# Kernel tuning notes

Measured on AMD Instinct MI355X. Metric: run time of the kernel, lower is better.

Reference implementation:

```python
import jax, jax.numpy as jnp
import numpy as np

TWO_PI = 2.0 * np.pi
SIGMA = 25.0  # marginal_prob_std sigma


def marginal_prob_std(t):
    # std(t) = sqrt((sigma^{2t} - 1) / (2 ln sigma)) for VE-SDE
    return jnp.sqrt((SIGMA ** (2.0 * t) - 1.0) / (2.0 * np.log(SIGMA)))


def edge_conv(x, src, dst, W1, b1, W2, b2, num_nodes):
    # PyG EdgeConv: msg = mlp(cat([x_i, x_j - x_i])), x_i = x[dst], x_j = x[src];
    # scatter-max over dst. First linear split so concat is never materialized:
    # cat([x_i, x_j - x_i]) @ W1 = x_i @ (Wa - Wb) + x_j @ Wb
    d = x.shape[-1]
    Wa, Wb = W1[:d], W1[d:]
    h_center = x @ (Wa - Wb)        # [N, H]
    h_nbr = x @ Wb                  # [N, H]
    e = jax.nn.relu(h_center[dst] + h_nbr[src] + b1)  # [E, H]
    e = e @ W2 + b2                 # [E, out]
    return jax.ops.segment_max(e, dst, num_segments=num_nodes)


def setup_inputs() -> dict:
    N, E, B, H, EM = 50000, 500000, 1024, 128, 64
    CLS, SD, GD, WD = 10, 4, 2, 2
    key = jax.random.key(0)
    ks = jax.random.split(key, 32)

    def lin(k, fi, fo):
        return jax.random.normal(k, (fi, fo), jnp.float32) / np.sqrt(fi)

    inp = {
        "t": jax.random.uniform(ks[0], (N, 1), jnp.float32, 1e-3, 1.0),
        "obj_x": jax.random.normal(ks[1], (N, SD), jnp.float32),
        "obj_geo": jax.random.normal(ks[2], (N, GD), jnp.float32),
        "wall": jax.random.normal(ks[3], (B, WD), jnp.float32),
        "category": jax.random.randint(ks[4], (N,), 0, CLS),
        "batch_idx": jnp.sort(jax.random.randint(ks[5], (N,), 0, B)),
        "src": jax.random.randint(ks[6], (E,), 0, N),
        "dst": jnp.tile(jnp.arange(N), E // N),  # every node receives edges
        "embed_W": jax.random.normal(ks[7], (CLS, EM), jnp.float32),
        "gfp_W": jax.random.normal(ks[8], (EM // 2,), jnp.float32) * 30.0,
        "sW": lin(ks[9], EM, EM), "sb": jnp.zeros((EM,), jnp.float32),
        "w1": lin(ks[10], WD, EM), "wb1": jnp.zeros((EM,), jnp.float32),
        "w2": lin(ks[11], EM, EM), "wb2": jnp.zeros((EM,), jnp.float32),
        "i1": lin(ks[12], SD + GD, H), "ib1": jnp.zeros((H,), jnp.float32),
        "i2": lin(ks[13], H, H), "ib2": jnp.zeros((H,), jnp.float32),
        "m1W1": lin(ks[14], 2 * (H + 3 * EM), H), "m1b1": jnp.zeros((H,), jnp.float32),
        "m1W2": lin(ks[15], H, H), "m1b2": jnp.zeros((H,), jnp.float32),
        "m2W1": lin(ks[16], 2 * (H + 3 * EM), H), "m2b1": jnp.zeros((H,), jnp.float32),
        "m2W2": lin(ks[17], H, SD), "m2b2": jnp.zeros((SD,), jnp.float32),
    }
    return inp


def reference(t, obj_x, obj_geo, wall, category, batch_idx, src, dst,
              embed_W, gfp_W, sW, sb, w1, wb1, w2, wb2,
              i1, ib1, i2, ib2, m1W1, m1b1, m1W2, m1b2,
              m2W1, m2b1, m2W2, m2b2):
    N = obj_x.shape[0]
    # conditioning features
    class_feat = jax.nn.relu(embed_W[category])                       # [N, EM]
    tv = t[:, 0]                                                      # [N]
    x_proj = tv[:, None] * gfp_W[None, :] * TWO_PI                    # [N, EM/2]
    gfp = jnp.concatenate([jnp.sin(x_proj), jnp.cos(x_proj)], axis=-1)
    sigma_feat = jax.nn.relu(gfp @ sW + sb)                           # [N, EM]
    wall_h = jax.nn.relu(jax.nn.relu(wall @ w1 + wb1) @ w2 + wb2)     # [B, EM]
    wall_feat = wall_h[batch_idx]                                     # [N, EM]
    cond = jnp.concatenate([class_feat, sigma_feat, wall_feat], axis=-1)

    # init encoder
    xin = jnp.concatenate([obj_x, obj_geo], axis=-1)                  # [N, 6]
    init = jax.nn.relu(jax.nn.relu(xin @ i1 + ib1) @ i2 + ib2)        # [N, H]

    # main backbone: two EdgeConvs with conditioning concat
    x = jnp.concatenate([init, cond], axis=-1)                        # [N, H+3EM]
    x = jax.nn.relu(edge_conv(x, src, dst, m1W1, m1b1, m1W2, m1b2, N))
    x = jnp.concatenate([x, cond], axis=-1)                           # [N, H+3EM]
    x = edge_conv(x, src, dst, m2W1, m2b1, m2W2, m2b2, N)             # [N, 4]

    return x / (marginal_prob_std(t) + 1e-7)
```

## Files before the change

kernel.cpp:

```cpp
#include <hip/hip_runtime.h>
#include <math.h>

#define NTHREADS 256
#define TWO_PI_F 6.28318530717958647692f
#define LOG_SIGMA 3.2188758248682006f

typedef unsigned short u16;
typedef unsigned int u32;
typedef short bf16x8 __attribute__((ext_vector_type(8)));
typedef float f32x4 __attribute__((ext_vector_type(4)));

#define MFMA(a, b, c) __builtin_amdgcn_mfma_f32_16x16x32_bf16((a), (b), (c), 0, 0, 0)

__device__ __forceinline__ u16 f2b(float f) {
  u32 u = __float_as_uint(f);
  u32 r = (u + 0x7fffu + ((u >> 16) & 1u)) >> 16;
  return (u16)r;
}
__device__ __forceinline__ float blo(u32 u) { return __uint_as_float(u << 16); }
__device__ __forceinline__ float bhi(u32 u) { return __uint_as_float(u & 0xffff0000u); }
__device__ __forceinline__ u32 pk(float lo, float hi) { return (u32)f2b(lo) | ((u32)f2b(hi) << 16); }

__global__ __launch_bounds__(256) void prep_kernel(
    const float* __restrict__ m1W2, const float* __restrict__ m1W1,
    const float* __restrict__ m2W1, const float* __restrict__ sW,
    const float* __restrict__ i1, const float* __restrict__ i2,
    u16* __restrict__ m1W2t, u16* __restrict__ Wc1t, u16* __restrict__ Wc2t,
    u16* __restrict__ sWt, u16* __restrict__ i1t, u16* __restrict__ i2t) {
  int idx = blockIdx.x * 256 + threadIdx.x;
  if (idx < 16384) {
    int n = idx >> 7, k = idx & 127;
    m1W2t[idx] = f2b(m1W2[k * 128 + n]);
  } else if (idx < 98304) {
    int j = idx - 16384;
    int n = j / 320, k = j - n * 320;
    float v = (n < 128) ? (m1W1[k * 128 + n] - m1W1[(320 + k) * 128 + n])
                        : m1W1[(320 + k) * 128 + (n - 128)];
    Wc1t[j] = f2b(v);
  } else if (idx < 180224) {
    int j = idx - 98304;
    int n = j / 320, k = j - n * 320;
    float v = (n < 128) ? (m2W1[k * 128 + n] - m2W1[(320 + k) * 128 + n])
                        : m2W1[(320 + k) * 128 + (n - 128)];
    Wc2t[j] = f2b(v);
  } else if (idx < 184320) {
    int j = idx - 180224;
    int n = j >> 6, k = j & 63;
    sWt[j] = f2b(sW[k * 64 + n]);
  } else if (idx < 188416) {
    int j = idx - 184320;
    int n = j >> 5, k = j & 31;
    i1t[j] = (k < 6) ? f2b(i1[k * 128 + n]) : (u16)0;
  } else if (idx < 204800) {
    int j = idx - 188416;
    int n = j >> 7, k = j & 127;
    i2t[j] = f2b(i2[k * 128 + n]);
  }
}

__global__ void wall_kernel(const float* __restrict__ wall,
                            const float* __restrict__ w1, const float* __restrict__ wb1,
                            const float* __restrict__ w2, const float* __restrict__ wb2,
                            float* __restrict__ wall_h) {
  __shared__ float h1[64];
  int b = blockIdx.x;
  int f = threadIdx.x;
  float v = wall[b * 2 + 0] * w1[f] + wall[b * 2 + 1] * w1[64 + f] + wb1[f];
  h1[f] = fmaxf(v, 0.f);
  __syncthreads();
  float acc = wb2[f];
  for (int k = 0; k < 64; ++k) acc = fmaf(h1[k], w2[k * 64 + f], acc);
  wall_h[b * 64 + f] = fmaxf(acc, 0.f);
}

__global__ __launch_bounds__(256) void node_kernel(
    const float* __restrict__ t, const float* __restrict__ obj_x,
    const float* __restrict__ obj_geo,
    const int* __restrict__ category, const int* __restrict__ batch_idx,
    const float* __restrict__ embed_W, const float* __restrict__ gfp_W,
    const u16* __restrict__ sWt, const float* __restrict__ sb,
    const u16* __restrict__ i1t, const float* __restrict__ ib1,
    const u16* __restrict__ i2t, const float* __restrict__ ib2,
    const u16* __restrict__ Wc1t, const float* __restrict__ m1b1,
    const float* __restrict__ wall_h,
    float* __restrict__ hc1, u16* __restrict__ hn1,
    u16* __restrict__ cond_bf, int N) {
  __shared__ u16 xb[64 * 328];
  __shared__ u16 ab[64 * 136];
  __shared__ float t_s[64];
  __shared__ int cat_s[64];
  __shared__ int bid_s[64];

  const int tid = threadIdx.x;
  const int base = blockIdx.x * 64;
  const int wave = tid >> 6, lane = tid & 63;
  const int ln16 = lane & 15, q8 = lane >> 4;

  bf16x8 bs0 = *(const bf16x8*)(sWt + (size_t)((wave * 16 + ln16) * 64) + q8 * 8);
  bf16x8 bs1 = *(const bf16x8*)(sWt + (size_t)((wave * 16 + ln16) * 64) + 32 + q8 * 8);
  bf16x8 bh[2];
#pragma unroll
  for (int nt = 0; nt < 2; ++nt)
    bh[nt] = *(const bf16x8*)(i1t + (size_t)((wave * 32 + nt * 16 + ln16) * 32) + q8 * 8);

  if (tid < 64) {
    int node = min(base + tid, N - 1);
    t_s[tid] = t[node];
    cat_s[tid] = category[node];
    bid_s[tid] = batch_idx[node];
  }
  __syncthreads();

  for (int idx = tid; idx < 64 * 32; idx += NTHREADS) {
    int row = idx >> 5, k = idx & 31;
    float xp = t_s[row] * gfp_W[k] * TWO_PI_F;
    float s, c;
    sincosf(xp, &s, &c);
    ab[row * 136 + k] = f2b(s);
    ab[row * 136 + 32 + k] = f2b(c);
  }
  for (int idx = tid; idx < 64 * 64; idx += NTHREADS) {
    int row = idx >> 6, f = idx & 63;
    xb[row * 328 + 128 + f] = f2b(fmaxf(embed_W[cat_s[row] * 64 + f], 0.f));
    xb[row * 328 + 256 + f] = f2b(wall_h[bid_s[row] * 64 + f]);
  }
  __syncthreads();

  f32x4 cs[4];
#pragma unroll
  for (int mt = 0; mt < 4; ++mt) cs[mt] = (f32x4)0.f;
#pragma unroll
  for (int mt = 0; mt < 4; ++mt) {
    bf16x8 a0 = *(const bf16x8*)&ab[(mt * 16 + ln16) * 136 + q8 * 8];
    cs[mt] = MFMA(a0, bs0, cs[mt]);
  }
#pragma unroll
  for (int mt = 0; mt < 4; ++mt) {
    bf16x8 a1 = *(const bf16x8*)&ab[(mt * 16 + ln16) * 136 + 32 + q8 * 8];
    cs[mt] = MFMA(a1, bs1, cs[mt]);
  }
  __syncthreads();

  {
    int col = wave * 16 + ln16;
    float bias = sb[col];
#pragma unroll
    for (int mt = 0; mt < 4; ++mt)
#pragma unroll
      for (int r = 0; r < 4; ++r)
        xb[(mt * 16 + q8 * 4 + r) * 328 + 192 + col] = f2b(fmaxf(cs[mt][r] + bias, 0.f));
  }
  for (int idx = tid; idx < 64 * 32; idx += NTHREADS) {
    int row = idx >> 5, k = idx & 31;
    int node = min(base + row, N - 1);
    float v = (k < 4) ? obj_x[node * 4 + k] : ((k < 6) ? obj_geo[node * 2 + (k - 4)] : 0.f);
    ab[row * 136 + k] = f2b(v);
  }
  __syncthreads();

  for (int idx = tid; idx < 64 * 24; idx += NTHREADS) {
    int row = idx / 24, q = idx - row * 24;
    int node = base + row;
    if (node < N)
      *(uint4*)&cond_bf[(size_t)node * 192 + q * 8] = *(uint4*)&xb[row * 328 + 128 + q * 8];
  }

  f32x4 ch[2][4];
#pragma unroll
  for (int nt = 0; nt < 2; ++nt)
#pragma unroll
    for (int mt = 0; mt < 4; ++mt) ch[nt][mt] = (f32x4)0.f;
#pragma unroll
  for (int mt = 0; mt < 4; ++mt) {
    bf16x8 a = *(const bf16x8*)&ab[(mt * 16 + ln16) * 136 + q8 * 8];
#pragma unroll
    for (int nt = 0; nt < 2; ++nt) ch[nt][mt] = MFMA(a, bh[nt], ch[nt][mt]);
  }
  bf16x8 bcur2[2], bnext2[2];
#pragma unroll
  for (int nt = 0; nt < 2; ++nt)
    bcur2[nt] = *(const bf16x8*)(i2t + (size_t)((wave * 32 + nt * 16 + ln16) * 128) + q8 * 8);
  __syncthreads();
#pragma unroll
  for (int nt = 0; nt < 2; ++nt) {
    int col = wave * 32 + nt * 16 + ln16;
    float bias = ib1[col];
#pragma unroll
    for (int mt = 0; mt < 4; ++mt)
#pragma unroll
      for (int r = 0; r < 4; ++r)
        ab[(mt * 16 + q8 * 4 + r) * 136 + col] = f2b(fmaxf(ch[nt][mt][r] + bias, 0.f));
  }
  __syncthreads();

  f32x4 ci[2][4];
#pragma unroll
  for (int nt = 0; nt < 2; ++nt)
#pragma unroll
    for (int mt = 0; mt < 4; ++mt) ci[nt][mt] = (f32x4)0.f;
  for (int kt = 0; kt < 4; ++kt) {
    if (kt < 3) {
#pragma unroll
      for (int nt = 0; nt < 2; ++nt)
        bnext2[nt] = *(const bf16x8*)(i2t + (size_t)((wave * 32 + nt * 16 + ln16) * 128) +
                                      (kt + 1) * 32 + q8 * 8);
    }
#pragma unroll
    for (int mt = 0; mt < 4; ++mt) {
      bf16x8 a = *(const bf16x8*)&ab[(mt * 16 + ln16) * 136 + kt * 32 + q8 * 8];
#pragma unroll
      for (int nt = 0; nt < 2; ++nt) ci[nt][mt] = MFMA(a, bcur2[nt], ci[nt][mt]);
    }
#pragma unroll
    for (int nt = 0; nt < 2; ++nt) bcur2[nt] = bnext2[nt];
  }
#pragma unroll
  for (int nt = 0; nt < 2; ++nt) {
    int col = wave * 32 + nt * 16 + ln16;
    float bias = ib2[col];
#pragma unroll
    for (int mt = 0; mt < 4; ++mt)
#pragma unroll
      for (int r = 0; r < 4; ++r)
        xb[(mt * 16 + q8 * 4 + r) * 328 + col] = f2b(fmaxf(ci[nt][mt][r] + bias, 0.f));
  }
  __syncthreads();

  f32x4 c2[4][4];
#pragma unroll
  for (int nt = 0; nt < 4; ++nt)
#pragma unroll
    for (int mt = 0; mt < 4; ++mt) c2[nt][mt] = (f32x4)0.f;
  bf16x8 bcur[4], bnext[4];
#pragma unroll
  for (int nt = 0; nt < 4; ++nt)
    bcur[nt] = *(const bf16x8*)(Wc1t + (size_t)((wave * 64 + nt * 16 + ln16) * 320) + q8 * 8);
  for (int kt = 0; kt < 10; ++kt) {
    if (kt < 9) {
#pragma unroll
      for (int nt = 0; nt < 4; ++nt)
        bnext[nt] = *(const bf16x8*)(Wc1t + (size_t)((wave * 64 + nt * 16 + ln16) * 320) +
                                     (kt + 1) * 32 + q8 * 8);
    }
#pragma unroll
    for (int mt = 0; mt < 4; ++mt) {
      bf16x8 a = *(const bf16x8*)&xb[(mt * 16 + ln16) * 328 + kt * 32 + q8 * 8];
#pragma unroll
      for (int nt = 0; nt < 4; ++nt) c2[nt][mt] = MFMA(a, bcur[nt], c2[nt][mt]);
    }
#pragma unroll
    for (int nt = 0; nt < 4; ++nt) bcur[nt] = bnext[nt];
  }
#pragma unroll
  for (int nt = 0; nt < 4; ++nt) {
    int col = wave * 64 + nt * 16 + ln16;
#pragma unroll
    for (int mt = 0; mt < 4; ++mt)
#pragma unroll
      for (int r = 0; r < 4; ++r) {
        int node = base + mt * 16 + q8 * 4 + r;
        if (node < N) {
          if (col < 128)
            hc1[(size_t)node * 128 + col] = c2[nt][mt][r] + m1b1[col];
          else
            hn1[(size_t)node * 128 + (col - 128)] = f2b(c2[nt][mt][r]);
        }
      }
  }
}

__global__ __launch_bounds__(256) void edge1_kernel(
    const float* __restrict__ hc1, const u16* __restrict__ hn1,
    const u16* __restrict__ cond_bf, const int* __restrict__ src,
    const u16* __restrict__ m1W2t, const float* __restrict__ m1b2,
    const u16* __restrict__ Wc2t, const float* __restrict__ m2b1,
    float* __restrict__ hc2, u16* __restrict__ hn2, int N) {
  __shared__ u16 a_lds[32 * 136];
  __shared__ u16 x2_lds[32 * 328];
  __shared__ int sid[320];

  const int tid = threadIdx.x;
  const int base = blockIdx.x * 32;
  const int wave = tid >> 6, lane = tid & 63;
  const int ln16 = lane & 15, q8 = lane >> 4;

  for (int idx = tid; idx < 320; idx += NTHREADS) {
    int e = idx >> 5, n = idx & 31;
    int node = min(base + n, N - 1);
    sid[idx] = src[node + e * N];
  }
  for (int idx = tid; idx < 768; idx += NTHREADS) {
    int n = idx / 24, q = idx - n * 24;
    int node = min(base + n, N - 1);
    *(uint4*)&x2_lds[n * 328 + 128 + q * 8] = *(const uint4*)&cond_bf[(size_t)node * 192 + q * 8];
  }
  const int ln = tid >> 3, kq = tid & 7;
  const int lnode = min(base + ln, N - 1);
  float hcr[16];
#pragma unroll
  for (int q = 0; q < 4; ++q) {
    float4 v = *(const float4*)&hc1[(size_t)lnode * 128 + kq * 16 + q * 4];
    hcr[q * 4 + 0] = v.x; hcr[q * 4 + 1] = v.y; hcr[q * 4 + 2] = v.z; hcr[q * 4 + 3] = v.w;
  }
  bf16x8 bfrag[2][4];
#pragma unroll
  for (int nt = 0; nt < 2; ++nt)
#pragma unroll
    for (int kt = 0; kt < 4; ++kt)
      bfrag[nt][kt] = *(const bf16x8*)(m1W2t + (size_t)((2 * wave + nt) * 16 + ln16) * 128 +
                                       kt * 32 + q8 * 8);

  f32x4 ymax[2][2];
#pragma unroll
  for (int mt = 0; mt < 2; ++mt)
#pragma unroll
    for (int nt = 0; nt < 2; ++nt)
#pragma unroll
      for (int r = 0; r < 4; ++r) ymax[mt][nt][r] = -3.0e38f;

  __syncthreads();

  int s = sid[ln];
  uint4 g0 = *(const uint4*)&hn1[(size_t)s * 128 + kq * 16];
  uint4 g1 = *(const uint4*)&hn1[(size_t)s * 128 + kq * 16 + 8];

  for (int e = 0; e < 10; ++e) {
    float a[16];
    a[0] = blo(g0.x); a[1] = bhi(g0.x); a[2] = blo(g0.y); a[3] = bhi(g0.y);
    a[4] = blo(g0.z); a[5] = bhi(g0.z); a[6] = blo(g0.w); a[7] = bhi(g0.w);
    a[8] = blo(g1.x); a[9] = bhi(g1.x); a[10] = blo(g1.y); a[11] = bhi(g1.y);
    a[12] = blo(g1.z); a[13] = bhi(g1.z); a[14] = blo(g1.w); a[15] = bhi(g1.w);
#pragma unroll
    for (int i = 0; i < 16; ++i) a[i] = fmaxf(hcr[i] + a[i], 0.f);
    uint4 o0, o1;
    o0.x = pk(a[0], a[1]); o0.y = pk(a[2], a[3]); o0.z = pk(a[4], a[5]); o0.w = pk(a[6], a[7]);
    o1.x = pk(a[8], a[9]); o1.y = pk(a[10], a[11]); o1.z = pk(a[12], a[13]); o1.w = pk(a[14], a[15]);
    *(uint4*)&a_lds[ln * 136 + kq * 16] = o0;
    *(uint4*)&a_lds[ln * 136 + kq * 16 + 8] = o1;
    if (e < 9) {
      s = sid[(e + 1) * 32 + ln];
      g0 = *(const uint4*)&hn1[(size_t)s * 128 + kq * 16];
      g1 = *(const uint4*)&hn1[(size_t)s * 128 + kq * 16 + 8];
    }
    __syncthreads();
    f32x4 c[2][2];
#pragma unroll
    for (int mt = 0; mt < 2; ++mt)
#pragma unroll
      for (int nt = 0; nt < 2; ++nt) c[mt][nt] = (f32x4)0.f;
#pragma unroll
    for (int kt = 0; kt < 4; ++kt) {
      bf16x8 a0 = *(const bf16x8*)&a_lds[ln16 * 136 + kt * 32 + q8 * 8];
      bf16x8 a1 = *(const bf16x8*)&a_lds[(16 + ln16) * 136 + kt * 32 + q8 * 8];
#pragma unroll
      for (int nt = 0; nt < 2; ++nt) {
        c[0][nt] = MFMA(a0, bfrag[nt][kt], c[0][nt]);
        c[1][nt] = MFMA(a1, bfrag[nt][kt], c[1][nt]);
      }
    }
#pragma unroll
    for (int mt = 0; mt < 2; ++mt)
#pragma unroll
      for (int nt = 0; nt < 2; ++nt)
#pragma unroll
        for (int r = 0; r < 4; ++r) ymax[mt][nt][r] = fmaxf(ymax[mt][nt][r], c[mt][nt][r]);
    __syncthreads();
  }

#pragma unroll
  for (int mt = 0; mt < 2; ++mt)
#pragma unroll
    for (int nt = 0; nt < 2; ++nt) {
      int col = (2 * wave + nt) * 16 + ln16;
      float bias = m1b2[col];
#pragma unroll
      for (int r = 0; r < 4; ++r) {
        int row = mt * 16 + q8 * 4 + r;
        x2_lds[row * 328 + col] = f2b(fmaxf(ymax[mt][nt][r] + bias, 0.f));
      }
    }
  __syncthreads();

  f32x4 c2[2][4];
#pragma unroll
  for (int mt = 0; mt < 2; ++mt)
#pragma unroll
    for (int nt = 0; nt < 4; ++nt) c2[mt][nt] = (f32x4)0.f;
  bf16x8 bcur[4], bnext[4];
#pragma unroll
  for (int nt = 0; nt < 4; ++nt)
    bcur[nt] = *(const bf16x8*)(Wc2t + (size_t)((wave * 4 + nt) * 16 + ln16) * 320 + q8 * 8);
  for (int kt = 0; kt < 10; ++kt) {
    if (kt < 9) {
#pragma unroll
      for (int nt = 0; nt < 4; ++nt)
        bnext[nt] = *(const bf16x8*)(Wc2t + (size_t)((wave * 4 + nt) * 16 + ln16) * 320 +
                                     (kt + 1) * 32 + q8 * 8);
    }
    bf16x8 a0 = *(const bf16x8*)&x2_lds[ln16 * 328 + kt * 32 + q8 * 8];
    bf16x8 a1 = *(const bf16x8*)&x2_lds[(16 + ln16) * 328 + kt * 32 + q8 * 8];
#pragma unroll
    for (int nt = 0; nt < 4; ++nt) {
      c2[0][nt] = MFMA(a0, bcur[nt], c2[0][nt]);
      c2[1][nt] = MFMA(a1, bcur[nt], c2[1][nt]);
    }
#pragma unroll
    for (int nt = 0; nt < 4; ++nt) bcur[nt] = bnext[nt];
  }
#pragma unroll
  for (int mt = 0; mt < 2; ++mt)
#pragma unroll
    for (int nt = 0; nt < 4; ++nt) {
      int col = (wave * 4 + nt) * 16 + ln16;
#pragma unroll
      for (int r = 0; r < 4; ++r) {
        int row = mt * 16 + q8 * 4 + r;
        int node = base + row;
        if (node < N) {
          if (wave < 2)
            hc2[(size_t)node * 128 + col] = c2[mt][nt][r] + m2b1[col];
          else
            hn2[(size_t)node * 128 + (col - 128)] = f2b(c2[mt][nt][r]);
        }
      }
    }
}

__global__ __launch_bounds__(256) void edge2_kernel(
    const float* __restrict__ hc2, const u16* __restrict__ hn2,
    const int* __restrict__ src, const float* __restrict__ t,
    const float* __restrict__ m2W2, const float* __restrict__ m2b2,
    float* __restrict__ out, int N) {
  const int tid = threadIdx.x;
  const int base = blockIdx.x * 32;
  const int ln = tid >> 3, kq = tid & 7;
  const int node = min(base + ln, N - 1);

  float hcr[16];
#pragma unroll
  for (int q = 0; q < 4; ++q) {
    float4 v = *(const float4*)&hc2[(size_t)node * 128 + kq * 16 + q * 4];
    hcr[q * 4 + 0] = v.x; hcr[q * 4 + 1] = v.y; hcr[q * 4 + 2] = v.z; hcr[q * 4 + 3] = v.w;
  }
  float w[16][4];
#pragma unroll
  for (int i = 0; i < 16; ++i) {
    float4 v = *(const float4*)&m2W2[(kq * 16 + i) * 4];
    w[i][0] = v.x; w[i][1] = v.y; w[i][2] = v.z; w[i][3] = v.w;
  }
  float ymax[4] = {-3.0e38f, -3.0e38f, -3.0e38f, -3.0e38f};

  int s = src[node];
  uint4 g0 = *(const uint4*)&hn2[(size_t)s * 128 + kq * 16];
  uint4 g1 = *(const uint4*)&hn2[(size_t)s * 128 + kq * 16 + 8];
  for (int e = 0; e < 10; ++e) {
    float a[16];
    a[0] = blo(g0.x); a[1] = bhi(g0.x); a[2] = blo(g0.y); a[3] = bhi(g0.y);
    a[4] = blo(g0.z); a[5] = bhi(g0.z); a[6] = blo(g0.w); a[7] = bhi(g0.w);
    a[8] = blo(g1.x); a[9] = bhi(g1.x); a[10] = blo(g1.y); a[11] = bhi(g1.y);
    a[12] = blo(g1.z); a[13] = bhi(g1.z); a[14] = blo(g1.w); a[15] = bhi(g1.w);
    if (e < 9) {
      s = src[node + (e + 1) * N];
      g0 = *(const uint4*)&hn2[(size_t)s * 128 + kq * 16];
      g1 = *(const uint4*)&hn2[(size_t)s * 128 + kq * 16 + 8];
    }
    float acc[4] = {0.f, 0.f, 0.f, 0.f};
#pragma unroll
    for (int i = 0; i < 16; ++i) {
      float av = fmaxf(hcr[i] + a[i], 0.f);
#pragma unroll
      for (int j = 0; j < 4; ++j) acc[j] = fmaf(av, w[i][j], acc[j]);
    }
#pragma unroll
    for (int mask = 1; mask <= 4; mask <<= 1)
#pragma unroll
      for (int j = 0; j < 4; ++j) acc[j] += __shfl_xor(acc[j], mask);
#pragma unroll
    for (int j = 0; j < 4; ++j) ymax[j] = fmaxf(ymax[j], acc[j]);
  }
  if (kq < 4 && base + ln < N) {
    float tv = t[node];
    float mps = sqrtf((expf(2.f * tv * LOG_SIGMA) - 1.f) * (1.f / (2.f * LOG_SIGMA)));
    out[(size_t)node * 4 + kq] = (ymax[kq] + m2b2[kq]) / (mps + 1e-7f);
  }
}

extern "C" void kernel_launch(void* const* d_in, const int* in_sizes, int n_in,
                              void* d_out, int out_size, void* d_ws, size_t ws_size,
                              hipStream_t stream) {
  const float* t = (const float*)d_in[0];
  const float* obj_x = (const float*)d_in[1];
  const float* obj_geo = (const float*)d_in[2];
  const float* wall = (const float*)d_in[3];
  const int* category = (const int*)d_in[4];
  const int* batch_idx = (const int*)d_in[5];
  const int* src = (const int*)d_in[6];
  const float* embed_W = (const float*)d_in[8];
  const float* gfp_W = (const float*)d_in[9];
  const float* sW = (const float*)d_in[10];
  const float* sb = (const float*)d_in[11];
  const float* w1 = (const float*)d_in[12];
  const float* wb1 = (const float*)d_in[13];
  const float* w2 = (const float*)d_in[14];
  const float* wb2 = (const float*)d_in[15];
  const float* i1 = (const float*)d_in[16];
  const float* ib1 = (const float*)d_in[17];
  const float* i2 = (const float*)d_in[18];
  const float* ib2 = (const float*)d_in[19];
  const float* m1W1 = (const float*)d_in[20];
  const float* m1b1 = (const float*)d_in[21];
  const float* m1W2 = (const float*)d_in[22];
  const float* m1b2 = (const float*)d_in[23];
  const float* m2W1 = (const float*)d_in[24];
  const float* m2b1 = (const float*)d_in[25];
  const float* m2W2 = (const float*)d_in[26];
  const float* m2b2 = (const float*)d_in[27];
  float* out = (float*)d_out;

  const int N = in_sizes[0];
  const int B = in_sizes[3] / 2;

  char* w = (char*)d_ws;
  float* wall_h = (float*)w; w += (size_t)B * 64 * 4;
  u16* cond_bf = (u16*)w;   w += (size_t)N * 192 * 2;
  float* hc1 = (float*)w;   w += (size_t)N * 128 * 4;
  u16* hn1 = (u16*)w;       w += (size_t)N * 128 * 2;
  float* hc2 = (float*)w;   w += (size_t)N * 128 * 4;
  u16* hn2 = (u16*)w;       w += (size_t)N * 128 * 2;
  u16* m1W2t = (u16*)w;     w += (size_t)128 * 128 * 2;
  u16* Wc1t = (u16*)w;      w += (size_t)256 * 320 * 2;
  u16* Wc2t = (u16*)w;      w += (size_t)256 * 320 * 2;
  u16* sWt = (u16*)w;       w += (size_t)64 * 64 * 2;
  u16* i1t = (u16*)w;       w += (size_t)128 * 32 * 2;
  u16* i2t = (u16*)w;       w += (size_t)128 * 128 * 2;

  prep_kernel<<<dim3(800), dim3(256), 0, stream>>>(m1W2, m1W1, m2W1, sW, i1, i2,
                                                   m1W2t, Wc1t, Wc2t, sWt, i1t, i2t);
  wall_kernel<<<dim3(B), dim3(64), 0, stream>>>(wall, w1, wb1, w2, wb2, wall_h);
  node_kernel<<<dim3((N + 63) / 64), dim3(NTHREADS), 0, stream>>>(
      t, obj_x, obj_geo, category, batch_idx, embed_W, gfp_W, sWt, sb,
      i1t, ib1, i2t, ib2, Wc1t, m1b1, wall_h, hc1, hn1, cond_bf, N);
  edge1_kernel<<<dim3((N + 31) / 32), dim3(NTHREADS), 0, stream>>>(
      hc1, hn1, cond_bf, src, m1W2t, m1b2, Wc2t, m2b1, hc2, hn2, N);
  edge2_kernel<<<dim3((N + 31) / 32), dim3(NTHREADS), 0, stream>>>(
      hc2, hn2, src, t, m2W2, m2b2, out, N);
}
```

Baseline: 285.4 us.

## Split edge1 edges across waves and build MFMA A-fragments in registers

The edge1 kernel is reorganised so each wave takes half of the 10 neighbour edges and half of the output columns. Each wave builds its bf16 A fragments directly in registers from the gathered neighbour features plus an LDS copy of the centre features. This removes the per-edge LDS staging of activations and the two block barriers per edge. The two edge halves are then merged with an LDS max on bf16 bit patterns, which is valid only because the values are non-negative after ReLU. In exchange, each wave pair gathers the same neighbour rows twice, roughly doubling gather traffic, and the occupancy hint of 2 blocks may put pressure on registers; float-to-bf16 rounding now uses the HIP intrinsic.

```diff
diff --git a/kernel.cpp b/kernel.cpp
--- a/kernel.cpp
+++ b/kernel.cpp
@@ -1,4 +1,5 @@
 #include <hip/hip_runtime.h>
+#include <hip/hip_bf16.h>
 #include <math.h>
 
 #define NTHREADS 256
@@ -9,17 +10,19 @@
 typedef unsigned int u32;
 typedef short bf16x8 __attribute__((ext_vector_type(8)));
 typedef float f32x4 __attribute__((ext_vector_type(4)));
+typedef u32 u32x4 __attribute__((ext_vector_type(4)));
 
 #define MFMA(a, b, c) __builtin_amdgcn_mfma_f32_16x16x32_bf16((a), (b), (c), 0, 0, 0)
 
 __device__ __forceinline__ u16 f2b(float f) {
-  u32 u = __float_as_uint(f);
-  u32 r = (u + 0x7fffu + ((u >> 16) & 1u)) >> 16;
-  return (u16)r;
+  __hip_bfloat16 h = __float2bfloat16(f);
+  return __builtin_bit_cast(u16, h);
+}
+__device__ __forceinline__ u32 pk2(float lo, float hi) {
+  return (u32)f2b(lo) | ((u32)f2b(hi) << 16);
 }
 __device__ __forceinline__ float blo(u32 u) { return __uint_as_float(u << 16); }
 __device__ __forceinline__ float bhi(u32 u) { return __uint_as_float(u & 0xffff0000u); }
-__device__ __forceinline__ u32 pk(float lo, float hi) { return (u32)f2b(lo) | ((u32)f2b(hi) << 16); }
 
 __global__ __launch_bounds__(256) void prep_kernel(
     const float* __restrict__ m1W2, const float* __restrict__ m1W1,
@@ -269,13 +272,13 @@
   }
 }
 
-__global__ __launch_bounds__(256) void edge1_kernel(
+__global__ __launch_bounds__(256, 2) void edge1_kernel(
     const float* __restrict__ hc1, const u16* __restrict__ hn1,
     const u16* __restrict__ cond_bf, const int* __restrict__ src,
     const u16* __restrict__ m1W2t, const float* __restrict__ m1b2,
     const u16* __restrict__ Wc2t, const float* __restrict__ m2b1,
     float* __restrict__ hc2, u16* __restrict__ hn2, int N) {
-  __shared__ u16 a_lds[32 * 136];
+  __shared__ float hc_lds[32 * 132];
   __shared__ u16 x2_lds[32 * 328];
   __shared__ int sid[320];
 
@@ -283,102 +286,133 @@
   const int base = blockIdx.x * 32;
   const int wave = tid >> 6, lane = tid & 63;
   const int ln16 = lane & 15, q8 = lane >> 4;
+  const int ch = wave & 1;
+  const int eh = wave >> 1;
+
+  bf16x8 bfrag[4][4];
+#pragma unroll
+  for (int nt = 0; nt < 4; ++nt)
+#pragma unroll
+    for (int kt = 0; kt < 4; ++kt)
+      bfrag[nt][kt] = *(const bf16x8*)(m1W2t +
+          (size_t)((ch * 64 + nt * 16 + ln16) * 128) + kt * 32 + q8 * 8);
 
   for (int idx = tid; idx < 320; idx += NTHREADS) {
     int e = idx >> 5, n = idx & 31;
-    int node = min(base + n, N - 1);
-    sid[idx] = src[node + e * N];
+    sid[idx] = src[min(base + n, N - 1) + e * N];
   }
   for (int idx = tid; idx < 768; idx += NTHREADS) {
     int n = idx / 24, q = idx - n * 24;
     int node = min(base + n, N - 1);
     *(uint4*)&x2_lds[n * 328 + 128 + q * 8] = *(const uint4*)&cond_bf[(size_t)node * 192 + q * 8];
   }
-  const int ln = tid >> 3, kq = tid & 7;
-  const int lnode = min(base + ln, N - 1);
-  float hcr[16];
-#pragma unroll
-  for (int q = 0; q < 4; ++q) {
-    float4 v = *(const float4*)&hc1[(size_t)lnode * 128 + kq * 16 + q * 4];
-    hcr[q * 4 + 0] = v.x; hcr[q * 4 + 1] = v.y; hcr[q * 4 + 2] = v.z; hcr[q * 4 + 3] = v.w;
-  }
-  bf16x8 bfrag[2][4];
-#pragma unroll
-  for (int nt = 0; nt < 2; ++nt)
-#pragma unroll
-    for (int kt = 0; kt < 4; ++kt)
-      bfrag[nt][kt] = *(const bf16x8*)(m1W2t + (size_t)((2 * wave + nt) * 16 + ln16) * 128 +
-                                       kt * 32 + q8 * 8);
-
-  f32x4 ymax[2][2];
+  for (int idx = tid; idx < 1024; idx += NTHREADS) {
+    int row = idx >> 5, q = idx & 31;
+    int node = min(base + row, N - 1);
+    *(float4*)&hc_lds[row * 132 + q * 4] = *(const float4*)&hc1[(size_t)node * 128 + q * 4];
+  }
+  __syncthreads();
+
+  const int e0 = eh * 5;
+  uint4 g[2][4], gn[2][4];
+  {
+    int s0 = sid[e0 * 32 + ln16];
+    int s1 = sid[e0 * 32 + 16 + ln16];
+#pragma unroll
+    for (int kt = 0; kt < 4; ++kt) {
+      g[0][kt] = *(const uint4*)&hn1[(size_t)s0 * 128 + kt * 32 + q8 * 8];
+      g[1][kt] = *(const uint4*)&hn1[(size_t)s1 * 128 + kt * 32 + q8 * 8];
+    }
+  }
+
+  f32x4 ymax[2][4];
 #pragma unroll
   for (int mt = 0; mt < 2; ++mt)
 #pragma unroll
-    for (int nt = 0; nt < 2; ++nt)
+    for (int nt = 0; nt < 4; ++nt)
 #pragma unroll
       for (int r = 0; r < 4; ++r) ymax[mt][nt][r] = -3.0e38f;
 
-  __syncthreads();
-
-  int s = sid[ln];
-  uint4 g0 = *(const uint4*)&hn1[(size_t)s * 128 + kq * 16];
-  uint4 g1 = *(const uint4*)&hn1[(size_t)s * 128 + kq * 16 + 8];
-
-  for (int e = 0; e < 10; ++e) {
-    float a[16];
-    a[0] = blo(g0.x); a[1] = bhi(g0.x); a[2] = blo(g0.y); a[3] = bhi(g0.y);
-    a[4] = blo(g0.z); a[5] = bhi(g0.z); a[6] = blo(g0.w); a[7] = bhi(g0.w);
-    a[8] = blo(g1.x); a[9] = bhi(g1.x); a[10] = blo(g1.y); a[11] = bhi(g1.y);
-    a[12] = blo(g1.z); a[13] = bhi(g1.z); a[14] = blo(g1.w); a[15] = bhi(g1.w);
-#pragma unroll
-    for (int i = 0; i < 16; ++i) a[i] = fmaxf(hcr[i] + a[i], 0.f);
-    uint4 o0, o1;
-    o0.x = pk(a[0], a[1]); o0.y = pk(a[2], a[3]); o0.z = pk(a[4], a[5]); o0.w = pk(a[6], a[7]);
-    o1.x = pk(a[8], a[9]); o1.y = pk(a[10], a[11]); o1.z = pk(a[12], a[13]); o1.w = pk(a[14], a[15]);
-    *(uint4*)&a_lds[ln * 136 + kq * 16] = o0;
-    *(uint4*)&a_lds[ln * 136 + kq * 16 + 8] = o1;
-    if (e < 9) {
-      s = sid[(e + 1) * 32 + ln];
-      g0 = *(const uint4*)&hn1[(size_t)s * 128 + kq * 16];
-      g1 = *(const uint4*)&hn1[(size_t)s * 128 + kq * 16 + 8];
-    }
-    __syncthreads();
-    f32x4 c[2][2];
+#pragma unroll 1
+  for (int e = 0; e < 5; ++e) {
+    if (e < 4) {
+      int s0 = sid[(e0 + e + 1) * 32 + ln16];
+      int s1 = sid[(e0 + e + 1) * 32 + 16 + ln16];
+#pragma unroll
+      for (int kt = 0; kt < 4; ++kt) {
+        gn[0][kt] = *(const uint4*)&hn1[(size_t)s0 * 128 + kt * 32 + q8 * 8];
+        gn[1][kt] = *(const uint4*)&hn1[(size_t)s1 * 128 + kt * 32 + q8 * 8];
+      }
+    }
+#pragma unroll
+    for (int mt = 0; mt < 2; ++mt) {
+      f32x4 c[4];
+#pragma unroll
+      for (int nt = 0; nt < 4; ++nt) c[nt] = (f32x4)0.f;
+#pragma unroll
+      for (int kt = 0; kt < 4; ++kt) {
+        const float* hp = &hc_lds[(mt * 16 + ln16) * 132 + kt * 32 + q8 * 8];
+        uint4 gv = g[mt][kt];
+        float a0 = fmaxf(hp[0] + blo(gv.x), 0.f);
+        float a1 = fmaxf(hp[1] + bhi(gv.x), 0.f);
+        float a2 = fmaxf(hp[2] + blo(gv.y), 0.f);
+        float a3 = fmaxf(hp[3] + bhi(gv.y), 0.f);
+        float a4 = fmaxf(hp[4] + blo(gv.z), 0.f);
+        float a5 = fmaxf(hp[5] + bhi(gv.z), 0.f);
+        float a6 = fmaxf(hp[6] + blo(gv.w), 0.f);
+        float a7 = fmaxf(hp[7] + bhi(gv.w), 0.f);
+        u32x4 aw;
+        aw.x = pk2(a0, a1);
+        aw.y = pk2(a2, a3);
+        aw.z = pk2(a4, a5);
+        aw.w = pk2(a6, a7);
+        bf16x8 af = __builtin_bit_cast(bf16x8, aw);
+#pragma unroll
+        for (int nt = 0; nt < 4; ++nt) c[nt] = MFMA(af, bfrag[nt][kt], c[nt]);
+      }
+#pragma unroll
+      for (int nt = 0; nt < 4; ++nt)
+#pragma unroll
+        for (int r = 0; r < 4; ++r) ymax[mt][nt][r] = fmaxf(ymax[mt][nt][r], c[nt][r]);
+    }
+    if (e < 4) {
+#pragma unroll
+      for (int mt = 0; mt < 2; ++mt)
+#pragma unroll
+        for (int kt = 0; kt < 4; ++kt) g[mt][kt] = gn[mt][kt];
+    }
+  }
+
+  __syncthreads();
+  if (eh == 0) {
 #pragma unroll
     for (int mt = 0; mt < 2; ++mt)
 #pragma unroll
-      for (int nt = 0; nt < 2; ++nt) c[mt][nt] = (f32x4)0.f;
-#pragma unroll
-    for (int kt = 0; kt < 4; ++kt) {
-      bf16x8 a0 = *(const bf16x8*)&a_lds[ln16 * 136 + kt * 32 + q8 * 8];
-      bf16x8 a1 = *(const bf16x8*)&a_lds[(16 + ln16) * 136 + kt * 32 + q8 * 8];
-#pragma unroll
-      for (int nt = 0; nt < 2; ++nt) {
-        c[0][nt] = MFMA(a0, bfrag[nt][kt], c[0][nt]);
-        c[1][nt] = MFMA(a1, bfrag[nt][kt], c[1][nt]);
+      for (int nt = 0; nt < 4; ++nt) {
+        int col = ch * 64 + nt * 16 + ln16;
+        float bias = m1b2[col];
+#pragma unroll
+        for (int r = 0; r < 4; ++r)
+          x2_lds[(mt * 16 + q8 * 4 + r) * 328 + col] = f2b(fmaxf(ymax[mt][nt][r] + bias, 0.f));
       }
-    }
+  }
+  __syncthreads();
+  if (eh == 1) {
 #pragma unroll
     for (int mt = 0; mt < 2; ++mt)
 #pragma unroll
-      for (int nt = 0; nt < 2; ++nt)
-#pragma unroll
-        for (int r = 0; r < 4; ++r) ymax[mt][nt][r] = fmaxf(ymax[mt][nt][r], c[mt][nt][r]);
-    __syncthreads();
-  }
-
-#pragma unroll
-  for (int mt = 0; mt < 2; ++mt)
-#pragma unroll
-    for (int nt = 0; nt < 2; ++nt) {
-      int col = (2 * wave + nt) * 16 + ln16;
-      float bias = m1b2[col];
-#pragma unroll
-      for (int r = 0; r < 4; ++r) {
-        int row = mt * 16 + q8 * 4 + r;
-        x2_lds[row * 328 + col] = f2b(fmaxf(ymax[mt][nt][r] + bias, 0.f));
+      for (int nt = 0; nt < 4; ++nt) {
+        int col = ch * 64 + nt * 16 + ln16;
+        float bias = m1b2[col];
+#pragma unroll
+        for (int r = 0; r < 4; ++r) {
+          int off = (mt * 16 + q8 * 4 + r) * 328 + col;
+          u16 mine = f2b(fmaxf(ymax[mt][nt][r] + bias, 0.f));
+          u16 cur = x2_lds[off];
+          x2_lds[off] = (mine > cur) ? mine : cur;
+        }
       }
-    }
+  }
   __syncthreads();
 
   f32x4 c2[2][4];
```

Result: slower. 367.2 us (+28.7%).

## Double-buffer edge activation tile in edge1 and prefetch gathers two edges ahead

Applied to the files above, without the earlier changes.

Splits the per-edge LDS activation buffer into two halves so the next edge's ReLU/pack and gather overlap the current edge's MFMA, cutting two barriers per iteration down to one raw s_barrier. Gathers are issued two edges ahead to hide global latency. It also swaps the manual float-to-bf16 rounding for the HIP intrinsic. This costs extra LDS and registers, and correctness now depends on the hand-placed waitcnt and barrier.

```diff
diff --git a/kernel.cpp b/kernel.cpp
--- a/kernel.cpp
+++ b/kernel.cpp
@@ -1,4 +1,5 @@
 #include <hip/hip_runtime.h>
+#include <hip/hip_bf16.h>
 #include <math.h>
 
 #define NTHREADS 256
@@ -13,13 +14,14 @@
 #define MFMA(a, b, c) __builtin_amdgcn_mfma_f32_16x16x32_bf16((a), (b), (c), 0, 0, 0)
 
 __device__ __forceinline__ u16 f2b(float f) {
-  u32 u = __float_as_uint(f);
-  u32 r = (u + 0x7fffu + ((u >> 16) & 1u)) >> 16;
-  return (u16)r;
+  __hip_bfloat16 h = __float2bfloat16(f);
+  return __builtin_bit_cast(u16, h);
+}
+__device__ __forceinline__ u32 pk2(float lo, float hi) {
+  return (u32)f2b(lo) | ((u32)f2b(hi) << 16);
 }
 __device__ __forceinline__ float blo(u32 u) { return __uint_as_float(u << 16); }
 __device__ __forceinline__ float bhi(u32 u) { return __uint_as_float(u & 0xffff0000u); }
-__device__ __forceinline__ u32 pk(float lo, float hi) { return (u32)f2b(lo) | ((u32)f2b(hi) << 16); }
 
 __global__ __launch_bounds__(256) void prep_kernel(
     const float* __restrict__ m1W2, const float* __restrict__ m1W1,
@@ -269,13 +271,29 @@
   }
 }
 
+__device__ __forceinline__ void pack_edge(u16* __restrict__ dst, const float* __restrict__ hcr,
+                                          uint4 g0, uint4 g1, int ln, int kq) {
+  float a[16];
+  a[0] = blo(g0.x); a[1] = bhi(g0.x); a[2] = blo(g0.y); a[3] = bhi(g0.y);
+  a[4] = blo(g0.z); a[5] = bhi(g0.z); a[6] = blo(g0.w); a[7] = bhi(g0.w);
+  a[8] = blo(g1.x); a[9] = bhi(g1.x); a[10] = blo(g1.y); a[11] = bhi(g1.y);
+  a[12] = blo(g1.z); a[13] = bhi(g1.z); a[14] = blo(g1.w); a[15] = bhi(g1.w);
+#pragma unroll
+  for (int i = 0; i < 16; ++i) a[i] = fmaxf(hcr[i] + a[i], 0.f);
+  uint4 o0, o1;
+  o0.x = pk2(a[0], a[1]); o0.y = pk2(a[2], a[3]); o0.z = pk2(a[4], a[5]); o0.w = pk2(a[6], a[7]);
+  o1.x = pk2(a[8], a[9]); o1.y = pk2(a[10], a[11]); o1.z = pk2(a[12], a[13]); o1.w = pk2(a[14], a[15]);
+  *(uint4*)&dst[ln * 136 + kq * 16] = o0;
+  *(uint4*)&dst[ln * 136 + kq * 16 + 8] = o1;
+}
+
 __global__ __launch_bounds__(256) void edge1_kernel(
     const float* __restrict__ hc1, const u16* __restrict__ hn1,
     const u16* __restrict__ cond_bf, const int* __restrict__ src,
     const u16* __restrict__ m1W2t, const float* __restrict__ m1b2,
     const u16* __restrict__ Wc2t, const float* __restrict__ m2b1,
     float* __restrict__ hc2, u16* __restrict__ hn2, int N) {
-  __shared__ u16 a_lds[32 * 136];
+  __shared__ u16 a_lds[2][32 * 136];
   __shared__ u16 x2_lds[32 * 328];
   __shared__ int sid[320];
 
@@ -320,29 +338,24 @@
 
   __syncthreads();
 
-  int s = sid[ln];
-  uint4 g0 = *(const uint4*)&hn1[(size_t)s * 128 + kq * 16];
-  uint4 g1 = *(const uint4*)&hn1[(size_t)s * 128 + kq * 16 + 8];
-
+  {
+    int s0 = sid[ln];
+    uint4 g0 = *(const uint4*)&hn1[(size_t)s0 * 128 + kq * 16];
+    uint4 g1 = *(const uint4*)&hn1[(size_t)s0 * 128 + kq * 16 + 8];
+    pack_edge(&a_lds[0][0], hcr, g0, g1, ln, kq);
+  }
+  uint4 g0n, g1n;
+  {
+    int s1 = sid[32 + ln];
+    g0n = *(const uint4*)&hn1[(size_t)s1 * 128 + kq * 16];
+    g1n = *(const uint4*)&hn1[(size_t)s1 * 128 + kq * 16 + 8];
+  }
+  asm volatile("s_waitcnt lgkmcnt(0)" ::: "memory");
+  __builtin_amdgcn_s_barrier();
+
+#pragma unroll 2
   for (int e = 0; e < 10; ++e) {
-    float a[16];
-    a[0] = blo(g0.x); a[1] = bhi(g0.x); a[2] = blo(g0.y); a[3] = bhi(g0.y);
-    a[4] = blo(g0.z); a[5] = bhi(g0.z); a[6] = blo(g0.w); a[7] = bhi(g0.w);
-    a[8] = blo(g1.x); a[9] = bhi(g1.x); a[10] = blo(g1.y); a[11] = bhi(g1.y);
-    a[12] = blo(g1.z); a[13] = bhi(g1.z); a[14] = blo(g1.w); a[15] = bhi(g1.w);
-#pragma unroll
-    for (int i = 0; i < 16; ++i) a[i] = fmaxf(hcr[i] + a[i], 0.f);
-    uint4 o0, o1;
-    o0.x = pk(a[0], a[1]); o0.y = pk(a[2], a[3]); o0.z = pk(a[4], a[5]); o0.w = pk(a[6], a[7]);
-    o1.x = pk(a[8], a[9]); o1.y = pk(a[10], a[11]); o1.z = pk(a[12], a[13]); o1.w = pk(a[14], a[15]);
-    *(uint4*)&a_lds[ln * 136 + kq * 16] = o0;
-    *(uint4*)&a_lds[ln * 136 + kq * 16 + 8] = o1;
-    if (e < 9) {
-      s = sid[(e + 1) * 32 + ln];
-      g0 = *(const uint4*)&hn1[(size_t)s * 128 + kq * 16];
-      g1 = *(const uint4*)&hn1[(size_t)s * 128 + kq * 16 + 8];
-    }
-    __syncthreads();
+    const u16* abuf = &a_lds[e & 1][0];
     f32x4 c[2][2];
 #pragma unroll
     for (int mt = 0; mt < 2; ++mt)
@@ -350,8 +363,8 @@
       for (int nt = 0; nt < 2; ++nt) c[mt][nt] = (f32x4)0.f;
 #pragma unroll
     for (int kt = 0; kt < 4; ++kt) {
-      bf16x8 a0 = *(const bf16x8*)&a_lds[ln16 * 136 + kt * 32 + q8 * 8];
-      bf16x8 a1 = *(const bf16x8*)&a_lds[(16 + ln16) * 136 + kt * 32 + q8 * 8];
+      bf16x8 a0 = *(const bf16x8*)&abuf[ln16 * 136 + kt * 32 + q8 * 8];
+      bf16x8 a1 = *(const bf16x8*)&abuf[(16 + ln16) * 136 + kt * 32 + q8 * 8];
 #pragma unroll
       for (int nt = 0; nt < 2; ++nt) {
         c[0][nt] = MFMA(a0, bfrag[nt][kt], c[0][nt]);
@@ -364,7 +377,17 @@
       for (int nt = 0; nt < 2; ++nt)
 #pragma unroll
         for (int r = 0; r < 4; ++r) ymax[mt][nt][r] = fmaxf(ymax[mt][nt][r], c[mt][nt][r]);
-    __syncthreads();
+
+    if (e < 9) {
+      pack_edge(&a_lds[(e + 1) & 1][0], hcr, g0n, g1n, ln, kq);
+      if (e < 8) {
+        int s = sid[(e + 2) * 32 + ln];
+        g0n = *(const uint4*)&hn1[(size_t)s * 128 + kq * 16];
+        g1n = *(const uint4*)&hn1[(size_t)s * 128 + kq * 16 + 8];
+      }
+      asm volatile("s_waitcnt lgkmcnt(0)" ::: "memory");
+      __builtin_amdgcn_s_barrier();
+    }
   }
 
 #pragma unroll
```

New measurement: 282.3 us. No clear change (-1.1%).

## Restructure edge1 to keep gathered rows in MFMA registers with LDS weights

Applied to the files above, without the earlier changes.

Edge1 now processes 64 nodes per block, and each wave owns 16 node rows. Gathered neighbor features are formed directly into MFMA A-fragments in registers rather than staged through LDS. This removes the per-edge __syncthreads pairs and the LDS round-trip. The m1W2 weight is staged once in swizzled LDS, and the gathers are double-buffered two edges ahead; the second GEMM now covers 4 m-tiles per wave. It also switches bf16 conversion to the HIP intrinsic and adds a launch bound of 2 blocks per CU. In exchange it raises register and LDS pressure and re-reads B fragments from LDS for every edge.

```diff
diff --git a/kernel.cpp b/kernel.cpp
--- a/kernel.cpp
+++ b/kernel.cpp
@@ -1,4 +1,5 @@
 #include <hip/hip_runtime.h>
+#include <hip/hip_bf16.h>
 #include <math.h>
 
 #define NTHREADS 256
@@ -9,17 +10,19 @@
 typedef unsigned int u32;
 typedef short bf16x8 __attribute__((ext_vector_type(8)));
 typedef float f32x4 __attribute__((ext_vector_type(4)));
+typedef u32 u32x4 __attribute__((ext_vector_type(4)));
 
 #define MFMA(a, b, c) __builtin_amdgcn_mfma_f32_16x16x32_bf16((a), (b), (c), 0, 0, 0)
 
 __device__ __forceinline__ u16 f2b(float f) {
-  u32 u = __float_as_uint(f);
-  u32 r = (u + 0x7fffu + ((u >> 16) & 1u)) >> 16;
-  return (u16)r;
+  __hip_bfloat16 h = __float2bfloat16(f);
+  return __builtin_bit_cast(u16, h);
+}
+__device__ __forceinline__ u32 pk2(float lo, float hi) {
+  return (u32)f2b(lo) | ((u32)f2b(hi) << 16);
 }
 __device__ __forceinline__ float blo(u32 u) { return __uint_as_float(u << 16); }
 __device__ __forceinline__ float bhi(u32 u) { return __uint_as_float(u & 0xffff0000u); }
-__device__ __forceinline__ u32 pk(float lo, float hi) { return (u32)f2b(lo) | ((u32)f2b(hi) << 16); }
 
 __global__ __launch_bounds__(256) void prep_kernel(
     const float* __restrict__ m1W2, const float* __restrict__ m1W1,
@@ -269,121 +272,124 @@
   }
 }
 
-__global__ __launch_bounds__(256) void edge1_kernel(
+__device__ __forceinline__ void edge_step(
+    uint4 (&G)[4], int e, const int* sid_lds, const u16* __restrict__ hn1,
+    const u16* b_lds, const float (&hcr)[4][8], f32x4 (&ymax)[8],
+    int myrow, int q8, int ln16, int swz) {
+  int s2 = 0;
+  const bool pf = (e + 2 < 10);
+  if (pf) s2 = sid_lds[(e + 2) * 64 + myrow];
+  bf16x8 af[4];
+#pragma unroll
+  for (int kt = 0; kt < 4; ++kt) {
+    uint4 gv = G[kt];
+    float a0 = fmaxf(hcr[kt][0] + blo(gv.x), 0.f);
+    float a1 = fmaxf(hcr[kt][1] + bhi(gv.x), 0.f);
+    float a2 = fmaxf(hcr[kt][2] + blo(gv.y), 0.f);
+    float a3 = fmaxf(hcr[kt][3] + bhi(gv.y), 0.f);
+    float a4 = fmaxf(hcr[kt][4] + blo(gv.z), 0.f);
+    float a5 = fmaxf(hcr[kt][5] + bhi(gv.z), 0.f);
+    float a6 = fmaxf(hcr[kt][6] + blo(gv.w), 0.f);
+    float a7 = fmaxf(hcr[kt][7] + bhi(gv.w), 0.f);
+    u32x4 aw;
+    aw.x = pk2(a0, a1); aw.y = pk2(a2, a3); aw.z = pk2(a4, a5); aw.w = pk2(a6, a7);
+    af[kt] = __builtin_bit_cast(bf16x8, aw);
+    if (pf) G[kt] = *(const uint4*)&hn1[(size_t)s2 * 128 + kt * 32 + q8 * 8];
+  }
+#pragma unroll
+  for (int nt = 0; nt < 8; ++nt) {
+    f32x4 c = (f32x4)0.f;
+#pragma unroll
+    for (int kt = 0; kt < 4; ++kt) {
+      bf16x8 bf = *(const bf16x8*)&b_lds[(nt * 16 + ln16) * 128 + ((kt * 32 + q8 * 8) ^ swz)];
+      c = MFMA(af[kt], bf, c);
+    }
+#pragma unroll
+    for (int r = 0; r < 4; ++r) ymax[nt][r] = fmaxf(ymax[nt][r], c[r]);
+  }
+}
+
+#define X2S 336
+
+__global__ __launch_bounds__(256, 2) void edge1_kernel(
     const float* __restrict__ hc1, const u16* __restrict__ hn1,
     const u16* __restrict__ cond_bf, const int* __restrict__ src,
     const u16* __restrict__ m1W2t, const float* __restrict__ m1b2,
     const u16* __restrict__ Wc2t, const float* __restrict__ m2b1,
     float* __restrict__ hc2, u16* __restrict__ hn2, int N) {
-  __shared__ u16 a_lds[32 * 136];
-  __shared__ u16 x2_lds[32 * 328];
-  __shared__ int sid[320];
+  __shared__ u16 b_lds[128 * 128];
+  __shared__ u16 x2_lds[64 * X2S];
+  __shared__ int sid_lds[640];
 
   const int tid = threadIdx.x;
-  const int base = blockIdx.x * 32;
+  const int base = blockIdx.x * 64;
   const int wave = tid >> 6, lane = tid & 63;
   const int ln16 = lane & 15, q8 = lane >> 4;
-
-  for (int idx = tid; idx < 320; idx += NTHREADS) {
-    int e = idx >> 5, n = idx & 31;
-    int node = min(base + n, N - 1);
-    sid[idx] = src[node + e * N];
-  }
-  for (int idx = tid; idx < 768; idx += NTHREADS) {
+  const int myrow = wave * 16 + ln16;
+  const int mynode = min(base + myrow, N - 1);
+  const int swz = (ln16 & 7) << 3;
+
+  for (int idx = tid; idx < 640; idx += NTHREADS) {
+    int e = idx >> 6, n = idx & 63;
+    sid_lds[idx] = src[min(base + n, N - 1) + e * N];
+  }
+  for (int idx = tid; idx < 2048; idx += NTHREADS) {
+    int j = idx * 8;
+    int row = j >> 7, col = j & 127;
+    *(uint4*)&b_lds[row * 128 + (col ^ ((row & 7) << 3))] = *(const uint4*)&m1W2t[j];
+  }
+  for (int idx = tid; idx < 1536; idx += NTHREADS) {
     int n = idx / 24, q = idx - n * 24;
     int node = min(base + n, N - 1);
-    *(uint4*)&x2_lds[n * 328 + 128 + q * 8] = *(const uint4*)&cond_bf[(size_t)node * 192 + q * 8];
-  }
-  const int ln = tid >> 3, kq = tid & 7;
-  const int lnode = min(base + ln, N - 1);
-  float hcr[16];
-#pragma unroll
-  for (int q = 0; q < 4; ++q) {
-    float4 v = *(const float4*)&hc1[(size_t)lnode * 128 + kq * 16 + q * 4];
-    hcr[q * 4 + 0] = v.x; hcr[q * 4 + 1] = v.y; hcr[q * 4 + 2] = v.z; hcr[q * 4 + 3] = v.w;
-  }
-  bf16x8 bfrag[2][4];
-#pragma unroll
-  for (int nt = 0; nt < 2; ++nt)
+    *(uint4*)&x2_lds[n * X2S + 128 + q * 8] = *(const uint4*)&cond_bf[(size_t)node * 192 + q * 8];
+  }
+  float hcr[4][8];
+#pragma unroll
+  for (int kt = 0; kt < 4; ++kt) {
+    float4 v0 = *(const float4*)&hc1[(size_t)mynode * 128 + kt * 32 + q8 * 8];
+    float4 v1 = *(const float4*)&hc1[(size_t)mynode * 128 + kt * 32 + q8 * 8 + 4];
+    hcr[kt][0] = v0.x; hcr[kt][1] = v0.y; hcr[kt][2] = v0.z; hcr[kt][3] = v0.w;
+    hcr[kt][4] = v1.x; hcr[kt][5] = v1.y; hcr[kt][6] = v1.z; hcr[kt][7] = v1.w;
+  }
+  __syncthreads();
+
+  f32x4 ymax[8];
+#pragma unroll
+  for (int nt = 0; nt < 8; ++nt)
+#pragma unroll
+    for (int r = 0; r < 4; ++r) ymax[nt][r] = -3.0e38f;
+
+  uint4 gA[4], gB[4];
+  {
+    int s0 = sid_lds[myrow];
+    int s1 = sid_lds[64 + myrow];
 #pragma unroll
     for (int kt = 0; kt < 4; ++kt)
-      bfrag[nt][kt] = *(const bf16x8*)(m1W2t + (size_t)((2 * wave + nt) * 16 + ln16) * 128 +
-                                       kt * 32 + q8 * 8);
-
-  f32x4 ymax[2][2];
-#pragma unroll
-  for (int mt = 0; mt < 2; ++mt)
-#pragma unroll
-    for (int nt = 0; nt < 2; ++nt)
-#pragma unroll
-      for (int r = 0; r < 4; ++r) ymax[mt][nt][r] = -3.0e38f;
-
-  __syncthreads();
-
-  int s = sid[ln];
-  uint4 g0 = *(const uint4*)&hn1[(size_t)s * 128 + kq * 16];
-  uint4 g1 = *(const uint4*)&hn1[(size_t)s * 128 + kq * 16 + 8];
-
-  for (int e = 0; e < 10; ++e) {
-    float a[16];
-    a[0] = blo(g0.x); a[1] = bhi(g0.x); a[2] = blo(g0.y); a[3] = bhi(g0.y);
-    a[4] = blo(g0.z); a[5] = bhi(g0.z); a[6] = blo(g0.w); a[7] = bhi(g0.w);
-    a[8] = blo(g1.x); a[9] = bhi(g1.x); a[10] = blo(g1.y); a[11] = bhi(g1.y);
-    a[12] = blo(g1.z); a[13] = bhi(g1.z); a[14] = blo(g1.w); a[15] = bhi(g1.w);
-#pragma unroll
-    for (int i = 0; i < 16; ++i) a[i] = fmaxf(hcr[i] + a[i], 0.f);
-    uint4 o0, o1;
-    o0.x = pk(a[0], a[1]); o0.y = pk(a[2], a[3]); o0.z = pk(a[4], a[5]); o0.w = pk(a[6], a[7]);
-    o1.x = pk(a[8], a[9]); o1.y = pk(a[10], a[11]); o1.z = pk(a[12], a[13]); o1.w = pk(a[14], a[15]);
-    *(uint4*)&a_lds[ln * 136 + kq * 16] = o0;
-    *(uint4*)&a_lds[ln * 136 + kq * 16 + 8] = o1;
-    if (e < 9) {
-      s = sid[(e + 1) * 32 + ln];
-      g0 = *(const uint4*)&hn1[(size_t)s * 128 + kq * 16];
-      g1 = *(const uint4*)&hn1[(size_t)s * 128 + kq * 16 + 8];
-    }
-    __syncthreads();
-    f32x4 c[2][2];
-#pragma unroll
-    for (int mt = 0; mt < 2; ++mt)
-#pragma unroll
-      for (int nt = 0; nt < 2; ++nt) c[mt][nt] = (f32x4)0.f;
-#pragma unroll
-    for (int kt = 0; kt < 4; ++kt) {
-      bf16x8 a0 = *(const bf16x8*)&a_lds[ln16 * 136 + kt * 32 + q8 * 8];
-      bf16x8 a1 = *(const bf16x8*)&a_lds[(16 + ln16) * 136 + kt * 32 + q8 * 8];
-#pragma unroll
-      for (int nt = 0; nt < 2; ++nt) {
-        c[0][nt] = MFMA(a0, bfrag[nt][kt], c[0][nt]);
-        c[1][nt] = MFMA(a1, bfrag[nt][kt], c[1][nt]);
-      }
-    }
-#pragma unroll
-    for (int mt = 0; mt < 2; ++mt)
-#pragma unroll
-      for (int nt = 0; nt < 2; ++nt)
-#pragma unroll
-        for (int r = 0; r < 4; ++r) ymax[mt][nt][r] = fmaxf(ymax[mt][nt][r], c[mt][nt][r]);
-    __syncthreads();
-  }
-
-#pragma unroll
-  for (int mt = 0; mt < 2; ++mt)
-#pragma unroll
-    for (int nt = 0; nt < 2; ++nt) {
-      int col = (2 * wave + nt) * 16 + ln16;
-      float bias = m1b2[col];
-#pragma unroll
-      for (int r = 0; r < 4; ++r) {
-        int row = mt * 16 + q8 * 4 + r;
-        x2_lds[row * 328 + col] = f2b(fmaxf(ymax[mt][nt][r] + bias, 0.f));
-      }
-    }
-  __syncthreads();
-
-  f32x4 c2[2][4];
-#pragma unroll
-  for (int mt = 0; mt < 2; ++mt)
+      gA[kt] = *(const uint4*)&hn1[(size_t)s0 * 128 + kt * 32 + q8 * 8];
+#pragma unroll
+    for (int kt = 0; kt < 4; ++kt)
+      gB[kt] = *(const uint4*)&hn1[(size_t)s1 * 128 + kt * 32 + q8 * 8];
+  }
+
+#pragma unroll
+  for (int ep = 0; ep < 5; ++ep) {
+    edge_step(gA, 2 * ep, sid_lds, hn1, b_lds, hcr, ymax, myrow, q8, ln16, swz);
+    edge_step(gB, 2 * ep + 1, sid_lds, hn1, b_lds, hcr, ymax, myrow, q8, ln16, swz);
+  }
+
+#pragma unroll
+  for (int nt = 0; nt < 8; ++nt) {
+    int col = nt * 16 + ln16;
+    float bias = m1b2[col];
+#pragma unroll
+    for (int r = 0; r < 4; ++r)
+      x2_lds[(wave * 16 + q8 * 4 + r) * X2S + col] = f2b(fmaxf(ymax[nt][r] + bias, 0.f));
+  }
+  __syncthreads();
+
+  f32x4 c2[4][4];
+#pragma unroll
+  for (int mt = 0; mt < 4; ++mt)
 #pragma unroll
     for (int nt = 0; nt < 4; ++nt) c2[mt][nt] = (f32x4)0.f;
   bf16x8 bcur[4], bnext[4];
@@ -397,25 +403,23 @@
         bnext[nt] = *(const bf16x8*)(Wc2t + (size_t)((wave * 4 + nt) * 16 + ln16) * 320 +
                                      (kt + 1) * 32 + q8 * 8);
     }
-    bf16x8 a0 = *(const bf16x8*)&x2_lds[ln16 * 328 + kt * 32 + q8 * 8];
-    bf16x8 a1 = *(const bf16x8*)&x2_lds[(16 + ln16) * 328 + kt * 32 + q8 * 8];
-#pragma unroll
-    for (int nt = 0; nt < 4; ++nt) {
-      c2[0][nt] = MFMA(a0, bcur[nt], c2[0][nt]);
-      c2[1][nt] = MFMA(a1, bcur[nt], c2[1][nt]);
+#pragma unroll
+    for (int mt = 0; mt < 4; ++mt) {
+      bf16x8 a = *(const bf16x8*)&x2_lds[(mt * 16 + ln16) * X2S + kt * 32 + q8 * 8];
+#pragma unroll
+      for (int nt = 0; nt < 4; ++nt) c2[mt][nt] = MFMA(a, bcur[nt], c2[mt][nt]);
     }
 #pragma unroll
     for (int nt = 0; nt < 4; ++nt) bcur[nt] = bnext[nt];
   }
 #pragma unroll
-  for (int mt = 0; mt < 2; ++mt)
+  for (int mt = 0; mt < 4; ++mt)
 #pragma unroll
     for (int nt = 0; nt < 4; ++nt) {
       int col = (wave * 4 + nt) * 16 + ln16;
 #pragma unroll
       for (int r = 0; r < 4; ++r) {
-        int row = mt * 16 + q8 * 4 + r;
-        int node = base + row;
+        int node = base + mt * 16 + q8 * 4 + r;
         if (node < N) {
           if (wave < 2)
             hc2[(size_t)node * 128 + col] = c2[mt][nt][r] + m2b1[col];
@@ -540,7 +544,7 @@
   node_kernel<<<dim3((N + 63) / 64), dim3(NTHREADS), 0, stream>>>(
       t, obj_x, obj_geo, category, batch_idx, embed_W, gfp_W, sWt, sb,
       i1t, ib1, i2t, ib2, Wc1t, m1b1, wall_h, hc1, hn1, cond_bf, N);
-  edge1_kernel<<<dim3((N + 31) / 32), dim3(NTHREADS), 0, stream>>>(
+  edge1_kernel<<<dim3((N + 63) / 64), dim3(NTHREADS), 0, stream>>>(
       hc1, hn1, cond_bf, src, m1W2t, m1b2, Wc2t, m2b1, hc2, hn2, N);
   edge2_kernel<<<dim3((N + 31) / 32), dim3(NTHREADS), 0, stream>>>(
       hc2, hn2, src, t, m2W2, m2b2, out, N);
```

Result: slower. 384.5 us (+34.7%).
